# Kernel tuning notes

Measured on AMD Instinct MI355X. Metric: run time of the kernel, lower is better.

## Reference

```python
import jax, jax.numpy as jnp
import numpy as np

C_QKV = 1024
C_HIDDEN = 64
NUM_HEADS = 16
INF = 1e9


def setup_inputs() -> dict:
    key = jax.random.key(0)
    ks = jax.random.split(key, 10)
    B, S = 2, 2048
    d = C_QKV
    hd = C_HIDDEN * NUM_HEADS
    sc = 0.02
    return {
        "input_qkv": jax.random.normal(ks[0], (B, S, d), jnp.float32),
        "mask": jnp.ones((B, 1, 1, S), jnp.float32),
        "bias": jax.random.normal(ks[1], (1, NUM_HEADS, S, S), jnp.float32) * sc,
        "wq": jax.random.normal(ks[2], (d, hd), jnp.float32) * sc,
        "wk": jax.random.normal(ks[3], (d, hd), jnp.float32) * sc,
        "wv": jax.random.normal(ks[4], (d, hd), jnp.float32) * sc,
        "wg": jax.random.normal(ks[5], (d, hd), jnp.float32) * sc,
        "bg": jnp.zeros((hd,), jnp.float32),
        "wo": jax.random.normal(ks[6], (hd, d), jnp.float32) * sc,
        "bo": jnp.zeros((d,), jnp.float32),
    }


def reference(input_qkv, mask, bias, wq, wk, wv, wg, bg, wo, bo):
    B, S, _ = input_qkv.shape
    H, C = NUM_HEADS, C_HIDDEN
    # projections -> [B, H, S, C]
    q = (input_qkv @ wq).reshape(B, S, H, C).transpose(0, 2, 1, 3)
    k = (input_qkv @ wk).reshape(B, S, H, C).transpose(0, 2, 1, 3)
    v = (input_qkv @ wv).reshape(B, S, H, C).transpose(0, 2, 1, 3)
    q = q / jnp.asarray(C, q.dtype) ** 0.5
    # scores [B, H, S, S] with additive mask and pair bias
    a = jnp.einsum("bhqc,bhkc->bhqk", q, k)
    a = a + (mask - 1.0) * INF + bias
    a = jax.nn.softmax(a, axis=-1)
    o = jnp.einsum("bhqk,bhkc->bhqc", a, v).transpose(0, 2, 1, 3)  # [B,S,H,C]
    gate = jax.nn.sigmoid(input_qkv @ wg + bg).reshape(B, S, H, C)
    o = (o * gate).reshape(B, S, H * C)
    return o @ wo + bo
```

## Files before the change

### kernel.cpp

```cpp
#include <hip/hip_runtime.h>
#include <hip/hip_bf16.h>
#include <stdint.h>

typedef unsigned short u16;
typedef __attribute__((ext_vector_type(8))) short short8;
typedef __attribute__((ext_vector_type(4))) short short4v;
typedef __attribute__((ext_vector_type(4))) float f32x4;

#define MFMA16 __builtin_amdgcn_mfma_f32_16x16x32_bf16

#define GLOAD_LDS16(gsrc, ldst) \
  __builtin_amdgcn_global_load_lds((const __attribute__((address_space(1))) void*)(gsrc), \
                                   (__attribute__((address_space(3))) void*)(ldst), 16, 0, 0)

__device__ __forceinline__ u16 f2bf(float x) {
  union { float f; uint32_t u; } v; v.f = x;
  uint32_t r = v.u + 0x7FFFu + ((v.u >> 16) & 1u);
  return (u16)(r >> 16);
}
__device__ __forceinline__ u16 f2bf_rn(float x) {
  __hip_bfloat16 h = __float2bfloat16(x);
  return *reinterpret_cast<u16*>(&h);
}
__device__ __forceinline__ float bf2f(u16 b) {
  union { uint32_t u; float f; } v; v.u = ((uint32_t)b) << 16;
  return v.f;
}

__global__ __launch_bounds__(256) void convert_bf16_kernel(
    const float* __restrict__ in, u16* __restrict__ out, int n) {
  int i = (blockIdx.x * 256 + threadIdx.x) * 8;
  if (i >= n) return;
  float4 a = *(const float4*)(in + i);
  float4 b = *(const float4*)(in + i + 4);
  short8 t;
  t[0] = (short)f2bf(a.x); t[1] = (short)f2bf(a.y);
  t[2] = (short)f2bf(a.z); t[3] = (short)f2bf(a.w);
  t[4] = (short)f2bf(b.x); t[5] = (short)f2bf(b.y);
  t[6] = (short)f2bf(b.z); t[7] = (short)f2bf(b.w);
  *(short8*)(out + i) = t;
}

__global__ __launch_bounds__(256) void transpose_w64_4(
    const float* __restrict__ w0, const float* __restrict__ w1,
    const float* __restrict__ w2, const float* __restrict__ w3,
    u16* __restrict__ WT) {
  __shared__ float tile[64][68];
  const int t = threadIdx.x;
  const int z = blockIdx.z;
  const float* W = (z == 0) ? w0 : (z == 1) ? w1 : (z == 2) ? w2 : w3;
  u16* dst_base = WT + (size_t)z * 1024 * 1024;
  const int k0 = blockIdx.x * 64, n0 = blockIdx.y * 64;
  {
    int r = t >> 2, c0 = (t & 3) * 16;
    const float* src = W + (size_t)(k0 + r) * 1024 + n0 + c0;
#pragma unroll
    for (int j = 0; j < 16; j += 4) {
      float4 v = *(const float4*)(src + j);
      tile[r][c0 + j + 0] = v.x; tile[r][c0 + j + 1] = v.y;
      tile[r][c0 + j + 2] = v.z; tile[r][c0 + j + 3] = v.w;
    }
  }
  __syncthreads();
  {
    int n = t >> 2, kq = (t & 3) * 16;
    short8 t0, t1;
#pragma unroll
    for (int j = 0; j < 8; ++j)  t0[j] = (short)f2bf(tile[kq + j][n]);
#pragma unroll
    for (int j = 0; j < 8; ++j)  t1[j] = (short)f2bf(tile[kq + 8 + j][n]);
    u16* dst = dst_base + (size_t)(n0 + n) * 1024 + k0 + kq;
    *(short8*)dst = t0;
    *(short8*)(dst + 8) = t1;
  }
}

__global__ __launch_bounds__(256) void transpose_w64(
    const float* __restrict__ W, u16* __restrict__ WT, int KK, int NN) {
  __shared__ float tile[64][68];
  const int t = threadIdx.x;
  const int k0 = blockIdx.x * 64, n0 = blockIdx.y * 64;
  {
    int r = t >> 2, c0 = (t & 3) * 16;
    const float* src = W + (size_t)(k0 + r) * NN + n0 + c0;
#pragma unroll
    for (int j = 0; j < 16; j += 4) {
      float4 v = *(const float4*)(src + j);
      tile[r][c0 + j + 0] = v.x; tile[r][c0 + j + 1] = v.y;
      tile[r][c0 + j + 2] = v.z; tile[r][c0 + j + 3] = v.w;
    }
  }
  __syncthreads();
  {
    int n = t >> 2, kq = (t & 3) * 16;
    short8 t0, t1;
#pragma unroll
    for (int j = 0; j < 8; ++j)  t0[j] = (short)f2bf(tile[kq + j][n]);
#pragma unroll
    for (int j = 0; j < 8; ++j)  t1[j] = (short)f2bf(tile[kq + 8 + j][n]);
    u16* dst = WT + (size_t)(n0 + n) * KK + k0 + kq;
    *(short8*)dst = t0;
    *(short8*)(dst + 8) = t1;
  }
}

__global__ __launch_bounds__(256) void transpose_v64(
    const u16* __restrict__ vin, u16* __restrict__ vout) {
  __shared__ u16 tile[64][80];
  const int t = threadIdx.x;
  const int s0 = blockIdx.x * 64;
  const int bh = blockIdx.y;
  const int b = bh >> 4, h = bh & 15;
  {
    int r = t >> 2, c0 = (t & 3) * 16;
    const u16* src = vin + (size_t)(b * 2048 + s0 + r) * 1024 + h * 64 + c0;
    *(short8*)&tile[r][c0] = *(const short8*)src;
    *(short8*)&tile[r][c0 + 8] = *(const short8*)(src + 8);
  }
  __syncthreads();
  {
    int c = t >> 2, s4 = (t & 3) * 16;
    short8 t0, t1;
#pragma unroll
    for (int j = 0; j < 8; ++j) t0[j] = (short)tile[s4 + j][c];
#pragma unroll
    for (int j = 0; j < 8; ++j) t1[j] = (short)tile[s4 + 8 + j][c];
    u16* dst = vout + (size_t)(bh * 64 + c) * 2048 + s0 + s4;
    *(short8*)dst = t0;
    *(short8*)(dst + 8) = t1;
  }
}

__global__ __launch_bounds__(256) void gemm_bt128(
    const u16* __restrict__ A, const u16* __restrict__ BTbase,
    void* __restrict__ dstbase, const float* __restrict__ bvec, int mode) {
  const int K = 1024;
  const int tid = threadIdx.x, lane = tid & 63, w = tid >> 6;
  const int wr = w >> 1, wc = w & 1;
  const int l15 = lane & 15, lg = lane >> 4;
  const int z = (mode < 0) ? (int)blockIdx.z : mode;
  const u16* BT = (mode < 0) ? BTbase + (size_t)z * 1024 * 1024 : BTbase;
  const int rbase = blockIdx.x * 128;
  const int nbase = blockIdx.y * 128;
  __shared__ u16 lsA[128 * 64];
  __shared__ u16 lsB[128 * 64];
  f32x4 acc[4][4] = {};
  const int col8 = (lane & 7) * 8;
  for (int kt = 0; kt < K / 64; ++kt) {
#pragma unroll
    for (int i = 0; i < 4; ++i) {
      int row = w * 32 + i * 8 + (lane >> 3);
      const u16* sa = A + (size_t)(rbase + row) * K + kt * 64 + col8;
      GLOAD_LDS16(sa, lsA + (w * 32 + i * 8) * 64 + lane * 8);
      const u16* sb = BT + (size_t)(nbase + row) * K + kt * 64 + col8;
      GLOAD_LDS16(sb, lsB + (w * 32 + i * 8) * 64 + lane * 8);
    }
    __syncthreads();
#pragma unroll
    for (int kk = 0; kk < 2; ++kk) {
      short8 af[4], bfr[4];
#pragma unroll
      for (int m = 0; m < 4; ++m)
        af[m] = *(const short8*)&lsA[(wr * 64 + m * 16 + l15) * 64 + kk * 32 + lg * 8];
#pragma unroll
      for (int n = 0; n < 4; ++n)
        bfr[n] = *(const short8*)&lsB[(wc * 64 + n * 16 + l15) * 64 + kk * 32 + lg * 8];
#pragma unroll
      for (int m = 0; m < 4; ++m)
#pragma unroll
        for (int n = 0; n < 4; ++n)
          acc[m][n] = MFMA16(af[m], bfr[n], acc[m][n], 0, 0, 0);
    }
    __syncthreads();
  }
  const int r0 = rbase + wr * 64;
  const int c0 = nbase + wc * 64;
  if (z == 4) {
    float* out = (float*)dstbase;
#pragma unroll
    for (int m = 0; m < 4; ++m)
#pragma unroll
      for (int n = 0; n < 4; ++n)
#pragma unroll
        for (int i = 0; i < 4; ++i) {
          int r = r0 + m * 16 + lg * 4 + i;
          int c = c0 + n * 16 + l15;
          out[(size_t)r * 1024 + c] = acc[m][n][i] + bvec[c];
        }
  } else {
    u16* dq = (u16*)dstbase + (size_t)z * 4096 * 1024;
#pragma unroll
    for (int m = 0; m < 4; ++m)
#pragma unroll
      for (int n = 0; n < 4; ++n)
#pragma unroll
        for (int i = 0; i < 4; ++i) {
          int r = r0 + m * 16 + lg * 4 + i;
          int c = c0 + n * 16 + l15;
          float v = acc[m][n][i];
          if (z == 0) v *= 0.125f;
          else if (z == 3) v = 1.f / (1.f + __expf(-(v + bvec[c])));
          dq[(size_t)r * 1024 + c] = f2bf(v);
        }
  }
}

__global__ __launch_bounds__(256, 2) void attn_kernel(
    const u16* __restrict__ qws, const u16* __restrict__ kws,
    const u16* __restrict__ vt, const u16* __restrict__ gws,
    const float* __restrict__ bias, const float* __restrict__ mask,
    u16* __restrict__ og) {
  const int tid = threadIdx.x;
  const int lane = tid & 63;
  const int w = tid >> 6;
  const int l15 = lane & 15, lg = lane >> 4;
  const int bx = blockIdx.x;
  const int qt = (bx & 7) | ((bx >> 4) << 3);
  const int b = (bx >> 3) & 1;
  const int h = blockIdx.y;

  __shared__ __align__(16) u16 ring[3][8192];
  __shared__ __align__(16) u16 lsP[4][2304];
  __shared__ __align__(16) u16 lsM[2048];

  const float* bias_base = bias + ((size_t)h * 2048 + qt * 128) * 2048;
  const u16* vt_base = vt + (size_t)((b * 16 + h) * 64) * 2048;
  const u16* k_base = kws + (size_t)(b * 2048) * 1024 + h * 64;

  {
    float4 m0 = *(const float4*)(mask + b * 2048 + tid * 8);
    float4 m1 = *(const float4*)(mask + b * 2048 + tid * 8 + 4);
    short8 mm;
    mm[0] = (short)f2bf((m0.x - 1.f) * 1e9f); mm[1] = (short)f2bf((m0.y - 1.f) * 1e9f);
    mm[2] = (short)f2bf((m0.z - 1.f) * 1e9f); mm[3] = (short)f2bf((m0.w - 1.f) * 1e9f);
    mm[4] = (short)f2bf((m1.x - 1.f) * 1e9f); mm[5] = (short)f2bf((m1.y - 1.f) * 1e9f);
    mm[6] = (short)f2bf((m1.z - 1.f) * 1e9f); mm[7] = (short)f2bf((m1.w - 1.f) * 1e9f);
    *(short8*)&lsM[tid * 8] = mm;
  }

  const size_t qrow0 = (size_t)(b * 2048 + qt * 128 + w * 32 + l15) * 1024 + h * 64;
  const size_t qrow1 = qrow0 + 16 * 1024;
  short8 qf00 = *(const short8*)(qws + qrow0 + lg * 8);
  short8 qf01 = *(const short8*)(qws + qrow0 + 32 + lg * 8);
  short8 qf10 = *(const short8*)(qws + qrow1 + lg * 8);
  short8 qf11 = *(const short8*)(qws + qrow1 + 32 + lg * 8);
  asm volatile("" :: "v"(qf00), "v"(qf01), "v"(qf10), "v"(qf11));
  asm volatile("s_waitcnt vmcnt(0)" ::: "memory");

  f32x4 O[2][4] = {};
  float lacc0 = 0.f, lacc1 = 0.f;
  f32x4 bA0, bA1, bA2, bA3, bA4, bA5, bA6, bA7;
  f32x4 bB0, bB1, bB2, bB3, bB4, bB5, bB6, bB7;

#define STAGE_KV(SLOT, KW) {                                                        \
    _Pragma("unroll") for (int it = 0; it < 2; ++it) {                              \
      int g_ = it * 256 + tid;                                                      \
      int r_ = g_ >> 3, cg_ = g_ & 7;                                               \
      GLOAD_LDS16(k_base + (size_t)((KW) * 64 + r_) * 1024 + ((cg_ ^ (r_ & 7)) * 8),\
                  &ring[SLOT][g_ * 8]);                                             \
      GLOAD_LDS16(vt_base + (size_t)r_ * 2048 + (KW) * 64 + ((cg_ ^ (r_ & 7)) * 8), \
                  &ring[SLOT][4096 + g_ * 8]);                                      \
    } }

#define BIAS_ISSUE(R0, R1, R2, R3, R4, R5, R6, R7, KW) {                            \
    const float* bp_ = bias_base + (size_t)(w * 32 + l15) * 2048 + (KW) * 64 + lg * 4; \
    asm volatile("global_load_dwordx4 %0, %1, off" : "=v"(R0) : "v"(bp_));          \
    asm volatile("global_load_dwordx4 %0, %1, off" : "=v"(R1) : "v"(bp_ + 16));     \
    asm volatile("global_load_dwordx4 %0, %1, off" : "=v"(R2) : "v"(bp_ + 32));     \
    asm volatile("global_load_dwordx4 %0, %1, off" : "=v"(R3) : "v"(bp_ + 48));     \
    asm volatile("global_load_dwordx4 %0, %1, off" : "=v"(R4) : "v"(bp_ + 16 * 2048)); \
    asm volatile("global_load_dwordx4 %0, %1, off" : "=v"(R5) : "v"(bp_ + 16 * 2048 + 16)); \
    asm volatile("global_load_dwordx4 %0, %1, off" : "=v"(R6) : "v"(bp_ + 16 * 2048 + 32)); \
    asm volatile("global_load_dwordx4 %0, %1, off" : "=v"(R7) : "v"(bp_ + 16 * 2048 + 48)); \
  }

#define COMPUTE(SLOT, KB, X0, X1, X2, X3, X4, X5, X6, X7) {                         \
    const u16* Kc_ = &ring[SLOT][0];                                                \
    const u16* Vc_ = &ring[SLOT][4096];                                             \
    f32x4 bb0[4] = {X0, X1, X2, X3};                                                \
    f32x4 bb1[4] = {X4, X5, X6, X7};                                                \
    f32x4 s_[2][4];                                                                 \
    _Pragma("unroll") for (int kt = 0; kt < 4; ++kt) {                              \
      int krow_ = kt * 16 + l15;                                                    \
      int sw_ = krow_ & 7;                                                          \
      short8 kfa_ = *(const short8*)&Kc_[(krow_ * 8 + (lg ^ sw_)) * 8];             \
      short8 kfb_ = *(const short8*)&Kc_[(krow_ * 8 + ((4 + lg) ^ sw_)) * 8];       \
      short4v mk_ = *(const short4v*)&lsM[(KB) * 64 + kt * 16 + lg * 4];            \
      f32x4 ci0_, ci1_;                                                             \
      _Pragma("unroll") for (int i = 0; i < 4; ++i) {                               \
        float m_ = bf2f((u16)mk_[i]);                                               \
        ci0_[i] = bb0[kt][i] + m_;                                                  \
        ci1_[i] = bb1[kt][i] + m_;                                                  \
      }                                                                             \
      s_[0][kt] = MFMA16(kfa_, qf00, ci0_, 0, 0, 0);                                \
      s_[0][kt] = MFMA16(kfb_, qf01, s_[0][kt], 0, 0, 0);                           \
      s_[1][kt] = MFMA16(kfa_, qf10, ci1_, 0, 0, 0);                                \
      s_[1][kt] = MFMA16(kfb_, qf11, s_[1][kt], 0, 0, 0);                           \
    }                                                                               \
    _Pragma("unroll") for (int kt = 0; kt < 4; ++kt) {                              \
      short4v p0_, p1_;                                                             \
      _Pragma("unroll") for (int i = 0; i < 4; ++i) {                               \
        float e0_ = __expf(s_[0][kt][i]); lacc0 += e0_; p0_[i] = (short)f2bf_rn(e0_); \
        float e1_ = __expf(s_[1][kt][i]); lacc1 += e1_; p1_[i] = (short)f2bf_rn(e1_); \
      }                                                                             \
      *(short4v*)&lsP[w][(l15) * 72 + kt * 16 + lg * 4] = p0_;                      \
      *(short4v*)&lsP[w][(16 + l15) * 72 + kt * 16 + lg * 4] = p1_;                 \
    }                                                                               \
    short8 pf00_ = *(const short8*)&lsP[w][(l15) * 72 + lg * 8];                    \
    short8 pf01_ = *(const short8*)&lsP[w][(l15) * 72 + 32 + lg * 8];               \
    short8 pf10_ = *(const short8*)&lsP[w][(16 + l15) * 72 + lg * 8];               \
    short8 pf11_ = *(const short8*)&lsP[w][(16 + l15) * 72 + 32 + lg * 8];          \
    _Pragma("unroll") for (int cf = 0; cf < 4; ++cf) {                              \
      int c_ = cf * 16 + l15;                                                       \
      int sw_ = c_ & 7;                                                             \
      short8 vf0_ = *(const short8*)&Vc_[(c_ * 8 + (lg ^ sw_)) * 8];                \
      short8 vf1_ = *(const short8*)&Vc_[(c_ * 8 + ((4 + lg) ^ sw_)) * 8];          \
      O[0][cf] = MFMA16(vf0_, pf00_, O[0][cf], 0, 0, 0);                            \
      O[0][cf] = MFMA16(vf1_, pf01_, O[0][cf], 0, 0, 0);                            \
      O[1][cf] = MFMA16(vf0_, pf10_, O[1][cf], 0, 0, 0);                            \
      O[1][cf] = MFMA16(vf1_, pf11_, O[1][cf], 0, 0, 0);                            \
    } }

#define BODY(KB, N, X0, X1, X2, X3, X4, X5, X6, X7) {                               \
    if ((KB) + 2 < 32) STAGE_KV(((KB) + 2) % 3, (KB) + 2);                          \
    COMPUTE((KB) % 3, KB, X0, X1, X2, X3, X4, X5, X6, X7);                          \
    if ((KB) + 2 < 32) BIAS_ISSUE(X0, X1, X2, X3, X4, X5, X6, X7, (KB) + 2);        \
    asm volatile("s_waitcnt vmcnt(" #N ")" ::: "memory");                           \
    asm volatile("s_waitcnt lgkmcnt(0)" ::: "memory");                              \
    __builtin_amdgcn_sched_barrier(0);                                              \
    __builtin_amdgcn_s_barrier(); }

  STAGE_KV(0, 0);
  BIAS_ISSUE(bA0, bA1, bA2, bA3, bA4, bA5, bA6, bA7, 0);
  STAGE_KV(1, 1);
  BIAS_ISSUE(bB0, bB1, bB2, bB3, bB4, bB5, bB6, bB7, 1);
  asm volatile("s_waitcnt vmcnt(12)" ::: "memory");
  asm volatile("s_waitcnt lgkmcnt(0)" ::: "memory");
  __builtin_amdgcn_sched_barrier(0);
  __builtin_amdgcn_s_barrier();

  for (int kb2 = 0; kb2 < 30; kb2 += 2) {
    BODY(kb2,     12, bA0, bA1, bA2, bA3, bA4, bA5, bA6, bA7);
    BODY(kb2 + 1, 12, bB0, bB1, bB2, bB3, bB4, bB5, bB6, bB7);
  }
  BODY(30, 0, bA0, bA1, bA2, bA3, bA4, bA5, bA6, bA7);
  BODY(31, 0, bB0, bB1, bB2, bB3, bB4, bB5, bB6, bB7);

  lacc0 += __shfl_xor(lacc0, 16); lacc0 += __shfl_xor(lacc0, 32);
  lacc1 += __shfl_xor(lacc1, 16); lacc1 += __shfl_xor(lacc1, 32);
  {
    float inv0 = 1.f / lacc0, inv1 = 1.f / lacc1;
#pragma unroll
    for (int cf = 0; cf < 4; ++cf) {
      short4v ga = *(const short4v*)(gws + qrow0 + cf * 16 + lg * 4);
      short4v gb = *(const short4v*)(gws + qrow1 + cf * 16 + lg * 4);
      short4v oa, ob;
#pragma unroll
      for (int i = 0; i < 4; ++i) {
        oa[i] = (short)f2bf_rn(O[0][cf][i] * inv0 * bf2f((u16)ga[i]));
        ob[i] = (short)f2bf_rn(O[1][cf][i] * inv1 * bf2f((u16)gb[i]));
      }
      *(short4v*)(og + qrow0 + cf * 16 + lg * 4) = oa;
      *(short4v*)(og + qrow1 + cf * 16 + lg * 4) = ob;
    }
  }
#undef STAGE_KV
#undef BIAS_ISSUE
#undef COMPUTE
#undef BODY
}

extern "C" void kernel_launch(void* const* d_in, const int* in_sizes, int n_in,
                              void* d_out, int out_size, void* d_ws, size_t ws_size,
                              hipStream_t stream) {
  const float* x    = (const float*)d_in[0];
  const float* mask = (const float*)d_in[1];
  const float* bias = (const float*)d_in[2];
  const float* wq   = (const float*)d_in[3];
  const float* wk   = (const float*)d_in[4];
  const float* wv   = (const float*)d_in[5];
  const float* wg   = (const float*)d_in[6];
  const float* bg   = (const float*)d_in[7];
  const float* wo   = (const float*)d_in[8];
  const float* bo   = (const float*)d_in[9];
  float* out = (float*)d_out;

  char* ws = (char*)d_ws;
  const size_t MB = 1ull << 20;
  u16* xb   = (u16*)(ws + 0);
  u16* wt   = (u16*)(ws + 8 * MB);
  u16* wot  = (u16*)(ws + 16 * MB);
  u16* proj = (u16*)(ws + 18 * MB);
  u16* vtp  = (u16*)(ws + 50 * MB);
  u16* og   = (u16*)(ws + 58 * MB);
  const size_t PSZ = (size_t)4096 * 1024;

  convert_bf16_kernel<<<2048, 256, 0, stream>>>(x, xb, 4096 * 1024);

  transpose_w64_4<<<dim3(16, 16, 4), 256, 0, stream>>>(wq, wk, wv, wg, wt);
  transpose_w64<<<dim3(16, 16), 256, 0, stream>>>(wo, wot, 1024, 1024);

  gemm_bt128<<<dim3(32, 8, 4), 256, 0, stream>>>(xb, wt, (void*)proj, bg, -1);

  transpose_v64<<<dim3(32, 32), 256, 0, stream>>>(proj + 2 * PSZ, vtp);

  attn_kernel<<<dim3(32, 16), 256, 0, stream>>>(proj, proj + PSZ, vtp, proj + 3 * PSZ,
                                                bias, mask, og);

  gemm_bt128<<<dim3(32, 8, 1), 256, 0, stream>>>(og, wot, (void*)out, bo, 4);
}
```

Before: 218.0 us.

## Stage K/V tiles through registers instead of direct global-to-LDS loads

Replaces the direct global_load_lds staging of K and V tiles with plain global loads into registers, double-buffered across iterations, followed by explicit swizzled LDS stores one iteration later. The LDS write and barrier now happen after the vmcnt wait, and the final iteration skips its barrier. The aim is to decouple global-load latency from the LDS ring and use wider, row-contiguous loads. In exchange it adds 32 VGPRs of staging registers and extra ds_write instructions, which may reduce occupancy or add LDS traffic.

```diff
diff --git a/kernel.cpp b/kernel.cpp
--- a/kernel.cpp
+++ b/kernel.cpp
@@ -246,21 +246,34 @@
   short8 qf11 = *(const short8*)(qws + qrow1 + 32 + lg * 8);
   asm volatile("" :: "v"(qf00), "v"(qf01), "v"(qf10), "v"(qf11));
   asm volatile("s_waitcnt vmcnt(0)" ::: "memory");
+  __builtin_amdgcn_sched_barrier(0);
 
   f32x4 O[2][4] = {};
   float lacc0 = 0.f, lacc1 = 0.f;
   f32x4 bA0, bA1, bA2, bA3, bA4, bA5, bA6, bA7;
   f32x4 bB0, bB1, bB2, bB3, bB4, bB5, bB6, bB7;
-
-#define STAGE_KV(SLOT, KW) {                                                        \
-    _Pragma("unroll") for (int it = 0; it < 2; ++it) {                              \
-      int g_ = it * 256 + tid;                                                      \
-      int r_ = g_ >> 3, cg_ = g_ & 7;                                               \
-      GLOAD_LDS16(k_base + (size_t)((KW) * 64 + r_) * 1024 + ((cg_ ^ (r_ & 7)) * 8),\
-                  &ring[SLOT][g_ * 8]);                                             \
-      GLOAD_LDS16(vt_base + (size_t)r_ * 2048 + (KW) * 64 + ((cg_ ^ (r_ & 7)) * 8), \
-                  &ring[SLOT][4096 + g_ * 8]);                                      \
-    } }
+  f32x4 kX0, kX1, vX0, vX1, kY0, kY1, vY0, vY1;
+
+#define STAGE_ISSUE(K0, K1, V0, V1, KW) {                                           \
+    int r_ = tid >> 3, cg_ = tid & 7;                                               \
+    const u16* kp_ = k_base + (size_t)((KW) * 64 + r_) * 1024 + cg_ * 8;            \
+    const u16* vp_ = vt_base + (size_t)r_ * 2048 + (KW) * 64 + cg_ * 8;             \
+    asm volatile("global_load_dwordx4 %0, %1, off" : "=v"(K0) : "v"(kp_));          \
+    asm volatile("global_load_dwordx4 %0, %1, off" : "=v"(K1) : "v"(kp_ + 32 * 1024)); \
+    asm volatile("global_load_dwordx4 %0, %1, off" : "=v"(V0) : "v"(vp_));          \
+    asm volatile("global_load_dwordx4 %0, %1, off" : "=v"(V1) : "v"(vp_ + 32 * 2048)); \
+  }
+
+#define STAGE_WRITE(SLOT, K0, K1, V0, V1) {                                         \
+    int r_ = tid >> 3, cg_ = tid & 7;                                               \
+    int d0_ = (r_ * 8 + (cg_ ^ (r_ & 7))) * 8;                                      \
+    int r2_ = r_ + 32;                                                              \
+    int d1_ = (r2_ * 8 + (cg_ ^ (r2_ & 7))) * 8;                                    \
+    *(f32x4*)&ring[SLOT][d0_] = K0;                                                 \
+    *(f32x4*)&ring[SLOT][d1_] = K1;                                                 \
+    *(f32x4*)&ring[SLOT][4096 + d0_] = V0;                                          \
+    *(f32x4*)&ring[SLOT][4096 + d1_] = V1;                                          \
+  }
 
 #define BIAS_ISSUE(R0, R1, R2, R3, R4, R5, R6, R7, KW) {                            \
     const float* bp_ = bias_base + (size_t)(w * 32 + l15) * 2048 + (KW) * 64 + lg * 4; \
@@ -321,30 +334,41 @@
       O[1][cf] = MFMA16(vf1_, pf11_, O[1][cf], 0, 0, 0);                            \
     } }
 
-#define BODY(KB, N, X0, X1, X2, X3, X4, X5, X6, X7) {                               \
-    if ((KB) + 2 < 32) STAGE_KV(((KB) + 2) % 3, (KB) + 2);                          \
+#define BODY(KB, N, SK0, SK1, SV0, SV1, TK0, TK1, TV0, TV1,                         \
+             X0, X1, X2, X3, X4, X5, X6, X7) {                                      \
+    if ((KB) + 2 < 32) STAGE_ISSUE(SK0, SK1, SV0, SV1, (KB) + 2);                   \
     COMPUTE((KB) % 3, KB, X0, X1, X2, X3, X4, X5, X6, X7);                          \
     if ((KB) + 2 < 32) BIAS_ISSUE(X0, X1, X2, X3, X4, X5, X6, X7, (KB) + 2);        \
     asm volatile("s_waitcnt vmcnt(" #N ")" ::: "memory");                           \
-    asm volatile("s_waitcnt lgkmcnt(0)" ::: "memory");                              \
     __builtin_amdgcn_sched_barrier(0);                                              \
-    __builtin_amdgcn_s_barrier(); }
-
-  STAGE_KV(0, 0);
+    if ((KB) + 1 < 32) {                                                            \
+      STAGE_WRITE(((KB) + 1) % 3, TK0, TK1, TV0, TV1);                              \
+      asm volatile("s_waitcnt lgkmcnt(0)" ::: "memory");                            \
+      __builtin_amdgcn_sched_barrier(0);                                            \
+      __builtin_amdgcn_s_barrier();                                                 \
+    } }
+
+  STAGE_ISSUE(kX0, kX1, vX0, vX1, 0);
   BIAS_ISSUE(bA0, bA1, bA2, bA3, bA4, bA5, bA6, bA7, 0);
-  STAGE_KV(1, 1);
+  STAGE_ISSUE(kY0, kY1, vY0, vY1, 1);
   BIAS_ISSUE(bB0, bB1, bB2, bB3, bB4, bB5, bB6, bB7, 1);
   asm volatile("s_waitcnt vmcnt(12)" ::: "memory");
+  __builtin_amdgcn_sched_barrier(0);
+  STAGE_WRITE(0, kX0, kX1, vX0, vX1);
   asm volatile("s_waitcnt lgkmcnt(0)" ::: "memory");
   __builtin_amdgcn_sched_barrier(0);
   __builtin_amdgcn_s_barrier();
 
   for (int kb2 = 0; kb2 < 30; kb2 += 2) {
-    BODY(kb2,     12, bA0, bA1, bA2, bA3, bA4, bA5, bA6, bA7);
-    BODY(kb2 + 1, 12, bB0, bB1, bB2, bB3, bB4, bB5, bB6, bB7);
-  }
-  BODY(30, 0, bA0, bA1, bA2, bA3, bA4, bA5, bA6, bA7);
-  BODY(31, 0, bB0, bB1, bB2, bB3, bB4, bB5, bB6, bB7);
+    BODY(kb2,     12, kX0, kX1, vX0, vX1, kY0, kY1, vY0, vY1,
+         bA0, bA1, bA2, bA3, bA4, bA5, bA6, bA7);
+    BODY(kb2 + 1, 12, kY0, kY1, vY0, vY1, kX0, kX1, vX0, vX1,
+         bB0, bB1, bB2, bB3, bB4, bB5, bB6, bB7);
+  }
+  BODY(30, 0, kX0, kX1, vX0, vX1, kY0, kY1, vY0, vY1,
+       bA0, bA1, bA2, bA3, bA4, bA5, bA6, bA7);
+  BODY(31, 0, kY0, kY1, vY0, vY1, kX0, kX1, vX0, vX1,
+       bB0, bB1, bB2, bB3, bB4, bB5, bB6, bB7);
 
   lacc0 += __shfl_xor(lacc0, 16); lacc0 += __shfl_xor(lacc0, 32);
   lacc1 += __shfl_xor(lacc1, 16); lacc1 += __shfl_xor(lacc1, 32);
@@ -364,7 +388,8 @@
       *(short4v*)(og + qrow1 + cf * 16 + lg * 4) = ob;
     }
   }
-#undef STAGE_KV
+#undef STAGE_ISSUE
+#undef STAGE_WRITE
 #undef BIAS_ISSUE
 #undef COMPUTE
 #undef BODY
```

Measured after the change: 207.5 us. -4.8%, faster.
